# Kernel tuning notes

Hardware: AMD Instinct MI355X
Metric: run time of the kernel (lower is better)

The kernel has to match this reference:

```python
import jax, jax.numpy as jnp
import numpy as np

H = W = 32
C = 512
RED = 16


def make_gus(v=1.5):
    # gus[p=(i,k), x, y] = exp(-((x-i)^2+(y-k)^2)/(2 v^2)) / (2 pi v^2), normalized per p.
    idx = np.arange(H, dtype=np.float64)
    d2 = (idx[:, None] - idx[None, :]) ** 2          # [center, coord]
    g1 = np.exp(-d2 / (2.0 * v * v))                  # separable factor
    g = np.einsum('ix,ky->ikxy', g1, g1) / (2.0 * np.pi * v * v)
    g = g / g.sum(axis=(2, 3), keepdims=True)         # per-position normalization
    return jnp.asarray(g.reshape(H * W, H, W), dtype=jnp.float32)


def setup_inputs() -> dict:
    key = jax.random.key(0)
    ks = jax.random.split(key, 6)
    b = 16
    return {
        'x': jax.random.normal(ks[0], (b, C, H, W), dtype=jnp.float32),
        'se_w1': jax.random.normal(ks[1], (C // RED, C), dtype=jnp.float32) * 0.02,
        'se_b1': jnp.zeros((C // RED,), dtype=jnp.float32),
        'se_w2': jax.random.normal(ks[2], (C, C // RED), dtype=jnp.float32) * 0.02,
        'se_b2': jnp.zeros((C,), dtype=jnp.float32),
        'down_w': jax.random.normal(ks[3], (C, 2 * C), dtype=jnp.float32) * 0.02,
        'gus': make_gus(1.5),
    }


def _patches3(img, h, w):
    # img: [b, c, h+2, w+2] -> [b, c, h, w, 9] (3x3 neighborhoods, row-major dy*3+dx)
    ps = [img[:, :, dy:dy + h, dx:dx + w] for dy in range(3) for dx in range(3)]
    return jnp.stack(ps, axis=-1)


def reference(x, se_w1, se_b1, se_w2, se_b2, down_w, gus):
    b, c, h, w = x.shape
    # --- SELayer ---
    s = x.mean(axis=(2, 3))                                   # [b, c]
    y = jax.nn.relu(s @ se_w1.T + se_b1)                       # [b, c/16]
    y = jax.nn.sigmoid(y @ se_w2.T + se_b2)                    # [b, c]
    out32 = x * y[:, :, None, None]
    # --- gaussian-weighted global pooling per output position ---
    # g[b, p, ch] = sum_{y,x} gus[p,y,x] * out32[b,ch,y,x]; then torch's view(c,h,w)
    gus_out = jnp.einsum('pyx,bcyx->bpc', gus, out32).reshape(b, c, h, w)
    # --- patch self-attention ---
    sig = jax.nn.sigmoid(out32)
    sigp = _patches3(jnp.pad(sig, ((0, 0), (0, 0), (1, 1), (1, 1))), h, w)    # [b,c,h,w,9]
    ffp = _patches3(jnp.pad(out32, ((0, 0), (0, 0), (1, 1), (1, 1))), h, w)   # [b,c,h,w,9]
    logits = jnp.einsum('bcyx,bcyxk->byxk', sig, sigp) / c     # mean over channels
    attn = jax.nn.softmax(logits, axis=-1)                     # softmax over 3x3 patch
    g2 = jnp.einsum('byxk,bcyxk->byxc', attn, ffp)             # [b,h,w,c] = [b, p, c]
    out_csa = g2.reshape(b, c, h, w)                           # torch view(c,h,w) of [hw,c]
    # --- down: 1x1 conv (no bias) + InstanceNorm2d + LeakyReLU(0.2) ---
    cat = jnp.concatenate([gus_out, out_csa], axis=1)          # [b, 2c, h, w]
    z = jnp.einsum('oi,biyx->boyx', down_w, cat)
    mu = z.mean(axis=(2, 3), keepdims=True)
    var = z.var(axis=(2, 3), keepdims=True)
    zn = (z - mu) * jax.lax.rsqrt(var + 1e-5)
    return jnp.where(zn >= 0, zn, 0.2 * zn)
```

## Files before the change

kernel.cpp:

```cpp
#include <hip/hip_runtime.h>
#include <stdint.h>

#define NB 16
#define NC 512
#define NS 1024
#define NR 32

typedef unsigned short u16;
typedef unsigned int u32;

typedef __attribute__((ext_vector_type(8))) short short8;
typedef __attribute__((ext_vector_type(4))) float f32x4;

__device__ __forceinline__ float bf2f(u16 u) {
    union { u32 i; float f; } c; c.i = ((u32)u) << 16; return c.f;
}
__device__ __forceinline__ u16 f2bf(float f) {
    union { float f; u32 i; } c; c.f = f;
    u32 r = (c.i + 0x7FFFu + ((c.i >> 16) & 1u)) >> 16;
    return (u16)r;
}
__device__ __forceinline__ float sigm(float x) {
    return 1.0f / (1.0f + __expf(-x));
}

__global__ void k_mean_cvt(const float* __restrict__ x, float* __restrict__ sm,
                           const float* __restrict__ g, const float* __restrict__ dw,
                           u16* __restrict__ gb, u16* __restrict__ dwb) {
    const int t = threadIdx.x;
    if (blockIdx.x < NB * NC) {
        const int row = blockIdx.x;
        const float4* xr = (const float4*)(x + (long)row * NS);
        float4 v = xr[t];
        float p = v.x + v.y + v.z + v.w;
        for (int off = 32; off; off >>= 1) p += __shfl_down(p, off);
        __shared__ __align__(16) float red[4];
        if ((t & 63) == 0) red[t >> 6] = p;
        __syncthreads();
        if (t == 0) sm[row] = (red[0] + red[1] + red[2] + red[3]) * (1.0f / 1024.0f);
    } else {
        const int i = (blockIdx.x - NB * NC) * 256 + t;
        gb[i] = f2bf(g[i]);
        if (i < 524288) dwb[i] = f2bf(dw[i]);
    }
}

__global__ void k_se(const float* __restrict__ sm, const float* __restrict__ w1,
                     const float* __restrict__ b1, const float* __restrict__ w2,
                     const float* __restrict__ b2, float* __restrict__ y) {
    const int b = blockIdx.x;
    __shared__ __align__(16) float s_s[NC];
    __shared__ __align__(16) float s_y1[NR];
    const int t = threadIdx.x;
    s_s[t] = sm[b * NC + t];
    s_s[t + 256] = sm[b * NC + t + 256];
    __syncthreads();
    {
        const int r = t >> 3, sub = t & 7;
        const float4* wr = (const float4*)(w1 + r * NC + sub * 64);
        const float4* sv = (const float4*)(s_s + sub * 64);
        float acc = 0.f;
#pragma unroll
        for (int i = 0; i < 16; ++i) {
            float4 wv = wr[i];
            float4 s4 = sv[i];
            acc += wv.x * s4.x + wv.y * s4.y + wv.z * s4.z + wv.w * s4.w;
        }
        acc += __shfl_down(acc, 4);
        acc += __shfl_down(acc, 2);
        acc += __shfl_down(acc, 1);
        if (sub == 0) s_y1[r] = fmaxf(acc + b1[r], 0.0f);
    }
    __syncthreads();
    for (int i = 0; i < 2; ++i) {
        int c = t + i * 256;
        float acc = b2[c];
#pragma unroll
        for (int r = 0; r < NR; ++r) acc += s_y1[r] * w2[c * NR + r];
        y[b * NC + c] = 1.0f / (1.0f + expf(-acc));
    }
}

__global__ void k_scale(const float* __restrict__ x, const float* __restrict__ y,
                        u16* __restrict__ o32, u16* __restrict__ o32t) {
    const int b = blockIdx.z;
    const int c0 = blockIdx.y * 32;
    const int s0 = blockIdx.x * 32;
    const int tx = threadIdx.x & 31, ty = threadIdx.x >> 5;
    __shared__ float tile[32][33];
    const float* xb = x + (long)b * NC * NS;
#pragma unroll
    for (int it = 0; it < 4; ++it) {
        int c = c0 + ty + it * 8;
        float v = xb[(long)c * NS + s0 + tx] * y[b * NC + c];
        tile[ty + it * 8][tx] = v;
        o32[((long)b * NC + c) * NS + s0 + tx] = f2bf(v);
    }
    __syncthreads();
#pragma unroll
    for (int it = 0; it < 4; ++it) {
        int sr = ty + it * 8;
        float tv = tile[tx][sr];
        long idx = ((long)b * NS + (s0 + sr)) * NC + c0 + tx;
        o32t[idx] = f2bf(tv);
    }
}

__device__ __forceinline__ void st_out(float* p, float v) { *p = v; }
__device__ __forceinline__ void st_out(u16* p, float v) { *p = f2bf(v); }

template <typename OT, bool BANDED>
__global__ __launch_bounds__(256)
void gemm_bt(const u16* __restrict__ A, const u16* __restrict__ Bt, OT* __restrict__ Co,
             int M, int N, int K, long batA, long batB, long batC, int ldc) {
    const int b = blockIdx.z;
    const u16* Ab = A + (long)b * batA;
    const u16* Bb = Bt + (long)b * batB;
    OT* Cb = Co + (long)b * batC;
    int m0, band;
    if (BANDED) { band = blockIdx.y & 1; m0 = (blockIdx.y >> 1) * 128; }
    else        { band = 0; m0 = blockIdx.y * 128; }
    const int n0 = blockIdx.x * 128;
    __shared__ __align__(16) u16 As[128 * 128];
    __shared__ __align__(16) u16 Bs[128 * 128];
    const int tid = threadIdx.x;
    const int lane = tid & 63, wave = tid >> 6;
    const int wm = (wave >> 1) * 64, wn = (wave & 1) * 64;
    f32x4 acc[4][4];
#pragma unroll
    for (int i = 0; i < 4; ++i)
#pragma unroll
        for (int j = 0; j < 4; ++j) acc[i][j] = (f32x4){0.f, 0.f, 0.f, 0.f};

    int srow[8], sg8[8];
#pragma unroll
    for (int r = 0; r < 8; ++r) {
        int c = r * 256 + tid;
        srow[r] = c >> 4;
        sg8[r] = ((c & 15) ^ (srow[r] & 15)) * 8;
    }

    for (int k0 = 0; k0 < K; k0 += 128) {
#pragma unroll
        for (int r = 0; r < 8; ++r) {
            const int c = r * 256 + tid;
            const u16* ga = Ab + (long)(m0 + srow[r]) * K + (k0 + sg8[r]);
            __builtin_amdgcn_global_load_lds(
                (const __attribute__((address_space(1))) u32*)ga,
                (__attribute__((address_space(3))) u32*)&As[c * 8], 16, 0, 0);
            const int brow = BANDED ? (2 * (n0 + srow[r]) + band) : (n0 + srow[r]);
            const u16* gb = Bb + (long)brow * K + (k0 + sg8[r]);
            __builtin_amdgcn_global_load_lds(
                (const __attribute__((address_space(1))) u32*)gb,
                (__attribute__((address_space(3))) u32*)&Bs[c * 8], 16, 0, 0);
        }
        __syncthreads();
#pragma unroll
        for (int kk = 0; kk < 128; kk += 32) {
            const int gq = (kk >> 3) + (lane >> 4);
            const int slot = gq ^ (lane & 15);
            short8 af[4], bfr[4];
#pragma unroll
            for (int i = 0; i < 4; ++i)
                af[i] = *(const short8*)&As[(wm + i * 16 + (lane & 15)) * 128 + slot * 8];
#pragma unroll
            for (int j = 0; j < 4; ++j)
                bfr[j] = *(const short8*)&Bs[(wn + j * 16 + (lane & 15)) * 128 + slot * 8];
#pragma unroll
            for (int i = 0; i < 4; ++i)
#pragma unroll
                for (int j = 0; j < 4; ++j)
                    acc[i][j] = __builtin_amdgcn_mfma_f32_16x16x32_bf16(af[i], bfr[j], acc[i][j], 0, 0, 0);
        }
        __syncthreads();
    }
    const int col = lane & 15, rq = (lane >> 4) * 4;
    const int crow0 = (BANDED ? band * 512 : 0) + m0 + wm;
#pragma unroll
    for (int i = 0; i < 4; ++i)
#pragma unroll
        for (int j = 0; j < 4; ++j)
#pragma unroll
            for (int r = 0; r < 4; ++r) {
                int row = crow0 + i * 16 + rq + r;
                int ncol = n0 + wn + j * 16 + col;
                st_out(&Cb[(long)row * ldc + ncol], acc[i][j][r]);
            }
}

__global__ __launch_bounds__(256)
void k_attn(const u16* __restrict__ o32t, u16* __restrict__ g2) {
    const int wave = threadIdx.x >> 6, lane = threadIdx.x & 63;
    const int tid = threadIdx.x;
    const int bx = blockIdx.x;
    const int b = blockIdx.y;
    const int y0 = bx >> 3;
    const int xbase = (bx & 7) * 4;
    const long base = (long)b * NS * NC;
    __shared__ __align__(16) u16 smem[2 * 18 * NC];

#pragma unroll
    for (int r = 0; r < 5; ++r) {
        int idx = r * 256 + tid;
        if (idx < 18 * 64) {
            int pair = idx >> 6;
            int ch0 = (idx & 63) * 8;
            int yy = y0 + pair / 6 - 1;
            int xx = xbase + pair % 6 - 1;
            short8 v = (short8){0, 0, 0, 0, 0, 0, 0, 0};
            short8 sv = (short8){0, 0, 0, 0, 0, 0, 0, 0};
            if (yy >= 0 && yy < 32 && xx >= 0 && xx < 32) {
                v = *(const short8*)&o32t[base + (long)(yy * 32 + xx) * NC + ch0];
#pragma unroll
                for (int j = 0; j < 8; ++j) sv[j] = (short)f2bf(sigm(bf2f((u16)v[j])));
            }
            *(short8*)&smem[(18 + pair) * NC + ch0] = v;
            *(short8*)&smem[pair * NC + ch0] = sv;
        }
    }
    __syncthreads();

    const int coff = lane * 8;
    short8 csv = *(const short8*)&smem[(6 + wave + 1) * NC + coff];
    float sc[8];
#pragma unroll
    for (int j = 0; j < 8; ++j) sc[j] = bf2f((u16)csv[j]);

    float part[9];
#pragma unroll
    for (int k = 0; k < 9; ++k) {
        int pair = (k / 3) * 6 + wave + k % 3;
        short8 sv = *(const short8*)&smem[pair * NC + coff];
        float p = 0.f;
#pragma unroll
        for (int j = 0; j < 8; ++j) p += sc[j] * bf2f((u16)sv[j]);
        part[k] = p;
    }
#pragma unroll
    for (int k = 0; k < 9; ++k)
        for (int off = 32; off; off >>= 1) part[k] += __shfl_down(part[k], off);

    if (lane == 0) {
        float mx = -1e30f;
#pragma unroll
        for (int k = 0; k < 9; ++k) { part[k] *= (1.0f / 512.0f); mx = fmaxf(mx, part[k]); }
        float sum = 0.f;
#pragma unroll
        for (int k = 0; k < 9; ++k) { part[k] = __expf(part[k] - mx); sum += part[k]; }
        float inv = 1.0f / sum;
#pragma unroll
        for (int k = 0; k < 9; ++k) part[k] *= inv;
    }
    float g[8] = {0.f, 0.f, 0.f, 0.f, 0.f, 0.f, 0.f, 0.f};
#pragma unroll
    for (int k = 0; k < 9; ++k) {
        float a = __shfl(part[k], 0);
        int pair = (k / 3) * 6 + wave + k % 3;
        short8 rv = *(const short8*)&smem[(18 + pair) * NC + coff];
#pragma unroll
        for (int j = 0; j < 8; ++j) g[j] += a * bf2f((u16)rv[j]);
    }
    short8 ov;
#pragma unroll
    for (int j = 0; j < 8; ++j) ov[j] = (short)f2bf(g[j]);
    const int s = y0 * 32 + xbase + wave;
    *(short8*)&g2[base + (long)s * NC + coff] = ov;
}

__global__ __launch_bounds__(256)
void k_tr(const u16* __restrict__ g2, u16* __restrict__ ct) {
    const int b = blockIdx.z;
    const int i0 = blockIdx.y * 64, s0 = blockIdx.x * 64;
    const int t = threadIdx.x;
    __shared__ __align__(16) u16 tile[64 * 64];
    const u16* src = g2 + (long)b * 524288 + (long)i0 * 1024;
#pragma unroll
    for (int it = 0; it < 2; ++it) {
        int c = it * 256 + t;
        int i = c >> 3, sg = c & 7;
        short8 v = *(const short8*)&src[(long)i * 1024 + s0 + sg * 8];
        int slot = sg ^ ((i >> 3) & 7);
        *(short8*)&tile[i * 64 + slot * 8] = v;
    }
    __syncthreads();
#pragma unroll
    for (int it = 0; it < 2; ++it) {
        int c = it * 256 + t;
        int srow = c >> 3, ig = c & 7;
        const int gs = srow >> 3, so = srow & 7;
        short8 v;
#pragma unroll
        for (int j = 0; j < 8; ++j) {
            int i = ig * 8 + j;
            int slot = gs ^ ig;
            v[j] = (short)tile[i * 64 + slot * 8 + so];
        }
        *(short8*)&ct[(long)b * 1048576 + (long)(s0 + srow) * 1024 + 512 + i0 + ig * 8] = v;
    }
}

__global__ void k_norm(const u16* __restrict__ z, float* __restrict__ out) {
    const int row = blockIdx.x;
    const int t = threadIdx.x;
    uint2 u = ((const uint2*)(z + (long)row * NS))[t];
    float v0 = bf2f((u16)(u.x & 0xffffu)), v1 = bf2f((u16)(u.x >> 16));
    float v2 = bf2f((u16)(u.y & 0xffffu)), v3 = bf2f((u16)(u.y >> 16));
    float sm = v0 + v1 + v2 + v3;
    float sq = v0 * v0 + v1 * v1 + v2 * v2 + v3 * v3;
    for (int off = 32; off; off >>= 1) { sm += __shfl_down(sm, off); sq += __shfl_down(sq, off); }
    __shared__ __align__(16) float rs[4], rq2[4];
    if ((t & 63) == 0) { rs[t >> 6] = sm; rq2[t >> 6] = sq; }
    __syncthreads();
    float tot = rs[0] + rs[1] + rs[2] + rs[3];
    float totq = rq2[0] + rq2[1] + rq2[2] + rq2[3];
    float mu = tot * (1.0f / 1024.0f);
    float var = totq * (1.0f / 1024.0f) - mu * mu;
    float sc = rsqrtf(var + 1e-5f);
    float4 o;
    float a;
    a = (v0 - mu) * sc; o.x = (a >= 0.f) ? a : 0.2f * a;
    a = (v1 - mu) * sc; o.y = (a >= 0.f) ? a : 0.2f * a;
    a = (v2 - mu) * sc; o.z = (a >= 0.f) ? a : 0.2f * a;
    a = (v3 - mu) * sc; o.w = (a >= 0.f) ? a : 0.2f * a;
    ((float4*)(out + (long)row * NS))[t] = o;
}

extern "C" void kernel_launch(void* const* d_in, const int* in_sizes, int n_in,
                              void* d_out, int out_size, void* d_ws, size_t ws_size,
                              hipStream_t stream) {
    const float* x   = (const float*)d_in[0];
    const float* w1  = (const float*)d_in[1];
    const float* b1  = (const float*)d_in[2];
    const float* w2  = (const float*)d_in[3];
    const float* b2  = (const float*)d_in[4];
    const float* dw  = (const float*)d_in[5];
    const float* gus = (const float*)d_in[6];
    float* out = (float*)d_out;
    char* ws = (char*)d_ws;

    float* sm_buf = (float*)(ws + 0);
    float* y_buf  = (float*)(ws + 32768);
    u16* gusbf    = (u16*)(ws + 65536);
    u16* dwbf     = (u16*)(ws + 2162688);
    u16* o32      = (u16*)(ws + 3211264);
    u16* o32t     = (u16*)(ws + 19988480);
    u16* g2b      = (u16*)(ws + 53542912);
    u16* catT     = (u16*)(ws + 19988480);
    u16* Z        = (u16*)(ws + 3211264);

    k_mean_cvt<<<dim3(NB * NC + 4096), dim3(256), 0, stream>>>(x, sm_buf, gus, dw, gusbf, dwbf);
    k_se<<<dim3(NB), dim3(256), 0, stream>>>(sm_buf, w1, b1, w2, b2, y_buf);
    k_scale<<<dim3(32, 16, NB), dim3(256), 0, stream>>>(x, y_buf, o32, o32t);
    k_attn<<<dim3(256, NB), dim3(256), 0, stream>>>(o32t, g2b);
    gemm_bt<u16, true><<<dim3(4, 8, NB), dim3(256), 0, stream>>>(
        o32, gusbf, catT, 512, 512, 1024, (long)NC * NS, 0L, (long)NS * 1024, 1024);
    k_tr<<<dim3(16, 8, NB), dim3(256), 0, stream>>>(g2b, catT);
    gemm_bt<u16, false><<<dim3(8, 4, NB), dim3(256), 0, stream>>>(
        dwbf, catT, Z, 512, 1024, 1024, 0L, (long)NS * 1024, (long)NC * NS, 1024);
    k_norm<<<dim3(NB * NC), dim3(256), 0, stream>>>(Z, out);
}
```

Measured before the change: 202.7 us.

## Fold gaussian pooling into down-projection weights and fuse into single GEMM

The gaussian pooling matrix is pre-multiplied into the first half of the 1x1 conv weights, giving a per-band weight matrix E that does not depend on the batch and is computed once. A single fused GEMM then takes E times the scaled input plus the conv weights times a reshuffled attention output, which removes the batched gus GEMM and the large concatenated intermediate. Total K per output drops from 2048 (1024 then 1024) to 1536 per batch. The cost is an extra small GEMM, a transpose kernel for gus, an uncoalesced strided-gather transpose for g2, and more bf16 rounding in the folded weights.

New measurement: 200.2 us. Within noise of the previous version (-1.3%).

```diff
diff --git a/kernel.cpp b/kernel.cpp
--- a/kernel.cpp
+++ b/kernel.cpp
@@ -25,8 +25,7 @@
 }
 
 __global__ void k_mean_cvt(const float* __restrict__ x, float* __restrict__ sm,
-                           const float* __restrict__ g, const float* __restrict__ dw,
-                           u16* __restrict__ gb, u16* __restrict__ dwb) {
+                           const float* __restrict__ dw, u16* __restrict__ dwb) {
     const int t = threadIdx.x;
     if (blockIdx.x < NB * NC) {
         const int row = blockIdx.x;
@@ -40,9 +39,36 @@
         if (t == 0) sm[row] = (red[0] + red[1] + red[2] + red[3]) * (1.0f / 1024.0f);
     } else {
         const int i = (blockIdx.x - NB * NC) * 256 + t;
-        gb[i] = f2bf(g[i]);
-        if (i < 524288) dwb[i] = f2bf(dw[i]);
-    }
+        dwb[i] = f2bf(dw[i]);
+    }
+}
+
+__global__ __launch_bounds__(256)
+void k_gusT(const float* __restrict__ g, u16* __restrict__ gt) {
+    const int p0 = (blockIdx.x & 15) * 64;
+    const int k0 = (blockIdx.x >> 4) * 64;
+    const int t = threadIdx.x;
+    __shared__ float tile[64][65];
+#pragma unroll
+    for (int it = 0; it < 4; ++it) {
+        int c = it * 256 + t;
+        int row = c >> 4;
+        int f4 = c & 15;
+        float4 v = *(const float4*)&g[(long)(p0 + row) * 1024 + k0 + f4 * 4];
+        tile[row][f4 * 4 + 0] = v.x; tile[row][f4 * 4 + 1] = v.y;
+        tile[row][f4 * 4 + 2] = v.z; tile[row][f4 * 4 + 3] = v.w;
+    }
+    __syncthreads();
+    const int q = t >> 7, k_loc = t & 63, h = (t >> 6) & 1;
+    short8 v0, v1;
+#pragma unroll
+    for (int jj = 0; jj < 8; ++jj) {
+        v0[jj] = (short)f2bf(tile[2 * (h * 16 + jj) + q][k_loc]);
+        v1[jj] = (short)f2bf(tile[2 * (h * 16 + 8 + jj) + q][k_loc]);
+    }
+    long ob = (long)q * 524288 + (long)(k0 + k_loc) * 512 + (p0 >> 1) + h * 16;
+    *(short8*)&gt[ob] = v0;
+    *(short8*)&gt[ob + 8] = v1;
 }
 
 __global__ void k_se(const float* __restrict__ sm, const float* __restrict__ w1,
@@ -106,20 +132,14 @@
     }
 }
 
-__device__ __forceinline__ void st_out(float* p, float v) { *p = v; }
-__device__ __forceinline__ void st_out(u16* p, float v) { *p = f2bf(v); }
-
-template <typename OT, bool BANDED>
 __global__ __launch_bounds__(256)
-void gemm_bt(const u16* __restrict__ A, const u16* __restrict__ Bt, OT* __restrict__ Co,
-             int M, int N, int K, long batA, long batB, long batC, int ldc) {
+void gemm_bt(const u16* __restrict__ A, const u16* __restrict__ Bt, u16* __restrict__ Co,
+             int K, long batA, long batB, long batC, int ldc, int lda, int ldb) {
     const int b = blockIdx.z;
     const u16* Ab = A + (long)b * batA;
     const u16* Bb = Bt + (long)b * batB;
-    OT* Cb = Co + (long)b * batC;
-    int m0, band;
-    if (BANDED) { band = blockIdx.y & 1; m0 = (blockIdx.y >> 1) * 128; }
-    else        { band = 0; m0 = blockIdx.y * 128; }
+    u16* Cb = Co + (long)b * batC;
+    const int m0 = blockIdx.y * 128;
     const int n0 = blockIdx.x * 128;
     __shared__ __align__(16) u16 As[128 * 128];
     __shared__ __align__(16) u16 Bs[128 * 128];
@@ -144,12 +164,11 @@
 #pragma unroll
         for (int r = 0; r < 8; ++r) {
             const int c = r * 256 + tid;
-            const u16* ga = Ab + (long)(m0 + srow[r]) * K + (k0 + sg8[r]);
+            const u16* ga = Ab + (long)(m0 + srow[r]) * lda + (k0 + sg8[r]);
             __builtin_amdgcn_global_load_lds(
                 (const __attribute__((address_space(1))) u32*)ga,
                 (__attribute__((address_space(3))) u32*)&As[c * 8], 16, 0, 0);
-            const int brow = BANDED ? (2 * (n0 + srow[r]) + band) : (n0 + srow[r]);
-            const u16* gb = Bb + (long)brow * K + (k0 + sg8[r]);
+            const u16* gb = Bb + (long)(n0 + srow[r]) * ldb + (k0 + sg8[r]);
             __builtin_amdgcn_global_load_lds(
                 (const __attribute__((address_space(1))) u32*)gb,
                 (__attribute__((address_space(3))) u32*)&Bs[c * 8], 16, 0, 0);
@@ -175,16 +194,98 @@
         __syncthreads();
     }
     const int col = lane & 15, rq = (lane >> 4) * 4;
-    const int crow0 = (BANDED ? band * 512 : 0) + m0 + wm;
 #pragma unroll
     for (int i = 0; i < 4; ++i)
 #pragma unroll
         for (int j = 0; j < 4; ++j)
 #pragma unroll
             for (int r = 0; r < 4; ++r) {
-                int row = crow0 + i * 16 + rq + r;
+                int row = m0 + wm + i * 16 + rq + r;
                 int ncol = n0 + wn + j * 16 + col;
-                st_out(&Cb[(long)row * ldc + ncol], acc[i][j][r]);
+                Cb[(long)row * ldc + ncol] = f2bf(acc[i][j][r]);
+            }
+}
+
+__global__ __launch_bounds__(256)
+void k_zgemm(const u16* __restrict__ Em, const u16* __restrict__ dwb,
+             const u16* __restrict__ o32, const u16* __restrict__ gsep,
+             u16* __restrict__ Z) {
+    const int b = blockIdx.z;
+    const int band = blockIdx.y & 1;
+    const int m0 = (blockIdx.y >> 1) * 128;
+    const int n0 = blockIdx.x * 128;
+    __shared__ __align__(16) u16 As[128 * 128];
+    __shared__ __align__(16) u16 Bs[128 * 128];
+    const int tid = threadIdx.x;
+    const int lane = tid & 63, wave = tid >> 6;
+    const int wm = (wave >> 1) * 64, wn = (wave & 1) * 64;
+    f32x4 acc[4][4];
+#pragma unroll
+    for (int i = 0; i < 4; ++i)
+#pragma unroll
+        for (int j = 0; j < 4; ++j) acc[i][j] = (f32x4){0.f, 0.f, 0.f, 0.f};
+
+    int srow[8], sg8[8];
+#pragma unroll
+    for (int r = 0; r < 8; ++r) {
+        int c = r * 256 + tid;
+        srow[r] = c >> 4;
+        sg8[r] = ((c & 15) ^ (srow[r] & 15)) * 8;
+    }
+    const u16* A0 = Em + (long)band * 524288;
+    const u16* B0 = o32 + (long)b * 524288;
+    const u16* B1 = gsep + (long)b * 524288 + (long)band * 262144;
+
+    for (int k0 = 0; k0 < 1536; k0 += 128) {
+#pragma unroll
+        for (int r = 0; r < 8; ++r) {
+            const int c = r * 256 + tid;
+            const u16* ga;
+            const u16* gb;
+            if (k0 < 1024) {
+                ga = A0 + (long)(m0 + srow[r]) * 1024 + (k0 + sg8[r]);
+                gb = B0 + (long)(n0 + srow[r]) * 1024 + (k0 + sg8[r]);
+            } else {
+                ga = dwb + (long)(m0 + srow[r]) * 1024 + 512 + (k0 - 1024) + sg8[r];
+                gb = B1 + (long)(n0 + srow[r]) * 512 + (k0 - 1024) + sg8[r];
+            }
+            __builtin_amdgcn_global_load_lds(
+                (const __attribute__((address_space(1))) u32*)ga,
+                (__attribute__((address_space(3))) u32*)&As[c * 8], 16, 0, 0);
+            __builtin_amdgcn_global_load_lds(
+                (const __attribute__((address_space(1))) u32*)gb,
+                (__attribute__((address_space(3))) u32*)&Bs[c * 8], 16, 0, 0);
+        }
+        __syncthreads();
+#pragma unroll
+        for (int kk = 0; kk < 128; kk += 32) {
+            const int gq = (kk >> 3) + (lane >> 4);
+            const int slot = gq ^ (lane & 15);
+            short8 af[4], bfr[4];
+#pragma unroll
+            for (int i = 0; i < 4; ++i)
+                af[i] = *(const short8*)&As[(wm + i * 16 + (lane & 15)) * 128 + slot * 8];
+#pragma unroll
+            for (int j = 0; j < 4; ++j)
+                bfr[j] = *(const short8*)&Bs[(wn + j * 16 + (lane & 15)) * 128 + slot * 8];
+#pragma unroll
+            for (int i = 0; i < 4; ++i)
+#pragma unroll
+                for (int j = 0; j < 4; ++j)
+                    acc[i][j] = __builtin_amdgcn_mfma_f32_16x16x32_bf16(af[i], bfr[j], acc[i][j], 0, 0, 0);
+        }
+        __syncthreads();
+    }
+    const int col = lane & 15, rq = (lane >> 4) * 4;
+#pragma unroll
+    for (int i = 0; i < 4; ++i)
+#pragma unroll
+        for (int j = 0; j < 4; ++j)
+#pragma unroll
+            for (int r = 0; r < 4; ++r) {
+                int row = m0 + wm + i * 16 + rq + r;
+                int ncol = n0 + wn + j * 16 + col;
+                Z[((long)b * 512 + row) * 1024 + band * 512 + ncol] = f2bf(acc[i][j][r]);
             }
 }
 
@@ -268,35 +369,23 @@
 }
 
 __global__ __launch_bounds__(256)
-void k_tr(const u16* __restrict__ g2, u16* __restrict__ ct) {
-    const int b = blockIdx.z;
-    const int i0 = blockIdx.y * 64, s0 = blockIdx.x * 64;
-    const int t = threadIdx.x;
-    __shared__ __align__(16) u16 tile[64 * 64];
-    const u16* src = g2 + (long)b * 524288 + (long)i0 * 1024;
-#pragma unroll
-    for (int it = 0; it < 2; ++it) {
-        int c = it * 256 + t;
-        int i = c >> 3, sg = c & 7;
-        short8 v = *(const short8*)&src[(long)i * 1024 + s0 + sg * 8];
-        int slot = sg ^ ((i >> 3) & 7);
-        *(short8*)&tile[i * 64 + slot * 8] = v;
-    }
-    __syncthreads();
-#pragma unroll
-    for (int it = 0; it < 2; ++it) {
-        int c = it * 256 + t;
-        int srow = c >> 3, ig = c & 7;
-        const int gs = srow >> 3, so = srow & 7;
-        short8 v;
-#pragma unroll
-        for (int j = 0; j < 8; ++j) {
-            int i = ig * 8 + j;
-            int slot = gs ^ ig;
-            v[j] = (short)tile[i * 64 + slot * 8 + so];
-        }
-        *(short8*)&ct[(long)b * 1048576 + (long)(s0 + srow) * 1024 + 512 + i0 + ig * 8] = v;
-    }
+void k_tr2(const u16* __restrict__ g2, u16* __restrict__ gs) {
+    long idx = (long)blockIdx.x * 256 + threadIdx.x;
+    int c = (int)(idx & 511);
+    int rest = (int)(idx >> 9);
+    int jc = rest & 31;
+    int q = (rest >> 5) & 1;
+    int b = rest >> 6;
+    const u16* src = g2 + (long)b * 524288;
+    short8 v0, v1;
+#pragma unroll
+    for (int jj = 0; jj < 8; ++jj) {
+        v0[jj] = (short)src[(long)(2 * (jc * 16 + jj) + q) * 512 + c];
+        v1[jj] = (short)src[(long)(2 * (jc * 16 + 8 + jj) + q) * 512 + c];
+    }
+    long ob = (long)b * 524288 + (long)q * 262144 + (long)c * 512 + jc * 16;
+    *(short8*)&gs[ob] = v0;
+    *(short8*)&gs[ob + 8] = v1;
 }
 
 __global__ void k_norm(const u16* __restrict__ z, float* __restrict__ out) {
@@ -340,22 +429,23 @@
 
     float* sm_buf = (float*)(ws + 0);
     float* y_buf  = (float*)(ws + 32768);
-    u16* gusbf    = (u16*)(ws + 65536);
-    u16* dwbf     = (u16*)(ws + 2162688);
-    u16* o32      = (u16*)(ws + 3211264);
-    u16* o32t     = (u16*)(ws + 19988480);
-    u16* g2b      = (u16*)(ws + 53542912);
-    u16* catT     = (u16*)(ws + 19988480);
-    u16* Z        = (u16*)(ws + 3211264);
-
-    k_mean_cvt<<<dim3(NB * NC + 4096), dim3(256), 0, stream>>>(x, sm_buf, gus, dw, gusbf, dwbf);
+    u16* dwbf     = (u16*)(ws + 65536);
+    u16* gusTb    = (u16*)(ws + 1114112);
+    u16* Ebuf     = (u16*)(ws + 3211264);
+    u16* o32      = (u16*)(ws + 5308416);
+    u16* o32t     = (u16*)(ws + 22085632);
+    u16* g2b      = (u16*)(ws + 38862848);
+    u16* g2sep    = (u16*)(ws + 22085632);
+    u16* Z        = (u16*)(ws + 38862848);
+
+    k_mean_cvt<<<dim3(NB * NC + 2048), dim3(256), 0, stream>>>(x, sm_buf, dw, dwbf);
+    k_gusT<<<dim3(256), dim3(256), 0, stream>>>(gus, gusTb);
     k_se<<<dim3(NB), dim3(256), 0, stream>>>(sm_buf, w1, b1, w2, b2, y_buf);
+    gemm_bt<<<dim3(8, 4, 2), dim3(256), 0, stream>>>(
+        dwbf, gusTb, Ebuf, 512, 0L, 524288L, 524288L, 1024, 1024, 512);
     k_scale<<<dim3(32, 16, NB), dim3(256), 0, stream>>>(x, y_buf, o32, o32t);
     k_attn<<<dim3(256, NB), dim3(256), 0, stream>>>(o32t, g2b);
-    gemm_bt<u16, true><<<dim3(4, 8, NB), dim3(256), 0, stream>>>(
-        o32, gusbf, catT, 512, 512, 1024, (long)NC * NS, 0L, (long)NS * 1024, 1024);
-    k_tr<<<dim3(16, 8, NB), dim3(256), 0, stream>>>(g2b, catT);
-    gemm_bt<u16, false><<<dim3(8, 4, NB), dim3(256), 0, stream>>>(
-        dwbf, catT, Z, 512, 1024, 1024, 0L, (long)NS * 1024, (long)NC * NS, 1024);
+    k_tr2<<<dim3(2048), dim3(256), 0, stream>>>(g2b, g2sep);
+    k_zgemm<<<dim3(4, 8, NB), dim3(256), 0, stream>>>(Ebuf, dwbf, o32, g2sep, Z);
     k_norm<<<dim3(NB * NC), dim3(256), 0, stream>>>(Z, out);
 }
```
